# Kernel tuning notes

Hardware: AMD Instinct MI355X
Metric: run time of the kernel (lower is better)

## Reference

```python
import jax, jax.numpy as jnp
import numpy as np

NT, C, B, N, H, E = 32768, 128, 64, 512, 4, 524288  # total nodes, channels, graphs, nodes/graph, heads, edges
DH = C // H
EPS = 1e-5


def batchnorm(x, g, b):
    # BatchNorm1d over the node dimension (training-mode batch statistics)
    m = x.mean(axis=0)
    v = x.var(axis=0)
    return (x - m) * jax.lax.rsqrt(v + EPS) * g + b


def setup_inputs() -> dict:
    key = jax.random.key(0)
    ks = jax.random.split(key, 8)
    s = 1.0 / np.sqrt(C)
    return dict(
        x=jax.random.normal(ks[0], (NT, C), jnp.float32),
        edge_index=jax.random.randint(ks[1], (2, E), 0, NT, dtype=jnp.int32),
        Wc=jax.random.normal(ks[2], (C, C), jnp.float32) * s,
        bc=jnp.zeros((C,), jnp.float32),
        in_proj_w=jax.random.normal(ks[3], (3 * C, C), jnp.float32) * s,
        in_proj_b=jnp.zeros((3 * C,), jnp.float32),
        out_proj_w=jax.random.normal(ks[4], (C, C), jnp.float32) * s,
        out_proj_b=jnp.zeros((C,), jnp.float32),
        gn1=jnp.ones((C,), jnp.float32), bn1=jnp.zeros((C,), jnp.float32),
        gn2=jnp.ones((C,), jnp.float32), bn2=jnp.zeros((C,), jnp.float32),
        gn3=jnp.ones((C,), jnp.float32), bn3=jnp.zeros((C,), jnp.float32),
        Wm1=jax.random.normal(ks[5], (2 * C, C), jnp.float32) * s,
        bm1=jnp.zeros((2 * C,), jnp.float32),
        Wm2=jax.random.normal(ks[6], (C, 2 * C), jnp.float32) / np.sqrt(2 * C),
        bm2=jnp.zeros((C,), jnp.float32),
    )


def reference(x, edge_index, Wc, bc, in_proj_w, in_proj_b, out_proj_w, out_proj_b,
              gn1, bn1, gn2, bn2, gn3, bn3, Wm1, bm1, Wm2, bm2):
    # --- local branch: mean-aggregation message passing + linear + residual + BN ---
    src, dst = edge_index[0], edge_index[1]
    agg = jax.ops.segment_sum(x[src], dst, num_segments=NT)            # [NT, C]
    cnt = jax.ops.segment_sum(jnp.ones((E, 1), x.dtype), dst, num_segments=NT)
    agg = agg / jnp.maximum(cnt, 1.0)
    h_local = agg @ Wc.T + bc + x                                       # dropout p=0 -> no-op
    h_local = batchnorm(h_local, gn1, bn1)

    # --- global branch: to_dense_batch (equal-size graphs -> reshape) + MHA ---
    hd = x.reshape(B, N, C)
    qkv = hd @ in_proj_w.T + in_proj_b                                  # [B, N, 3C]
    q, k, v = jnp.split(qkv, 3, axis=-1)
    q = q.reshape(B, N, H, DH).transpose(0, 2, 1, 3)                    # [B, H, N, DH]
    k = k.reshape(B, N, H, DH).transpose(0, 2, 1, 3)
    v = v.reshape(B, N, H, DH).transpose(0, 2, 1, 3)
    scores = jnp.einsum('bhqd,bhkd->bhqk', q, k) / np.sqrt(DH)          # [B, H, N, N]
    attn = jax.nn.softmax(scores, axis=-1)
    o = jnp.einsum('bhqk,bhkd->bhqd', attn, v)                          # [B, H, N, DH]
    o = o.transpose(0, 2, 1, 3).reshape(B, N, C)
    h_attn = (o @ out_proj_w.T + out_proj_b).reshape(NT, C) + x
    h_attn = batchnorm(h_attn, gn2, bn2)

    # --- combine + MLP + final norm ---
    out = h_local + h_attn
    out = out + (jax.nn.relu(out @ Wm1.T + bm1) @ Wm2.T + bm2)
    return batchnorm(out, gn3, bn3)
```

## Files before the change

kernel.cpp:

```cpp
#include <hip/hip_runtime.h>
#include <cstddef>

#define NT    32768
#define CCH   128
#define BB    64
#define NNODE 512
#define NHEAD 4
#define DHEAD 32
#define EE    524288
#define EPS   1e-5f
#define MAXDEG 96

typedef unsigned short u16;
typedef unsigned int   u32;
typedef __attribute__((ext_vector_type(8))) short short8;
typedef __attribute__((ext_vector_type(4))) short short4v;
typedef __attribute__((ext_vector_type(4))) float f32x4;

__device__ __forceinline__ float b2f(u32 w) { return __uint_as_float(w << 16); }
__device__ __forceinline__ u16 f2b(float f) {
    u32 u = __float_as_uint(f);
    u += 0x7FFF + ((u >> 16) & 1);
    return (u16)(u >> 16);
}

__global__ __launch_bounds__(256) void prep_kernel(const float* __restrict__ x,
                                                   const float* __restrict__ Wc,
                                                   const float* __restrict__ Wqkv,
                                                   const float* __restrict__ Wo,
                                                   const float* __restrict__ Wm1,
                                                   const float* __restrict__ Wm2,
                                                   u16* __restrict__ xb,
                                                   u16* __restrict__ Wcb,
                                                   u16* __restrict__ Wqkvb,
                                                   u16* __restrict__ Wob,
                                                   u16* __restrict__ Wm1b,
                                                   u16* __restrict__ Wm2b,
                                                   const int* __restrict__ ei,
                                                   int* __restrict__ cursor,
                                                   int* __restrict__ bucket) {
    if (blockIdx.x >= 2120) {
        int e = (blockIdx.x - 2120) * 256 + threadIdx.x;
        int src = ei[e];
        int dst = ei[EE + e];
        int pos = atomicAdd(cursor + dst, 1);
        if (pos < MAXDEG) bucket[dst * MAXDEG + pos] = src;
        return;
    }
    int r = blockIdx.x * 256 + threadIdx.x;
    const float* src; u16* dst;
    if (r < 524288) { src = x; dst = xb; }
    else if ((r -= 524288) < 2048) { src = Wc; dst = Wcb; }
    else if ((r -= 2048) < 6144) { src = Wqkv; dst = Wqkvb; }
    else if ((r -= 6144) < 2048) { src = Wo; dst = Wob; }
    else if ((r -= 2048) < 4096) { src = Wm1; dst = Wm1b; }
    else { r -= 4096; src = Wm2; dst = Wm2b; }
    size_t base = (size_t)r * 8;
    float4 a = *(const float4*)(src + base);
    float4 b = *(const float4*)(src + base + 4);
    uint4 u;
    u.x = (u32)f2b(a.x) | ((u32)f2b(a.y) << 16);
    u.y = (u32)f2b(a.z) | ((u32)f2b(a.w) << 16);
    u.z = (u32)f2b(b.x) | ((u32)f2b(b.y) << 16);
    u.w = (u32)f2b(b.z) | ((u32)f2b(b.w) << 16);
    *(uint4*)(dst + base) = u;
}

__global__ __launch_bounds__(256) void stage2_kernel(const int* __restrict__ bucket,
                                                     const int* __restrict__ cursor,
                                                     const u16* __restrict__ xb,
                                                     u16* __restrict__ aggb,
                                                     const u16* __restrict__ Wqkvb,
                                                     const float* __restrict__ bqkv,
                                                     u16* __restrict__ qkvb) {
    __shared__ __align__(16) char smem[26624];
    int tid = threadIdx.x;
    if (blockIdx.x < 4096) {
        int* srcs = (int*)smem;
        int ln = tid >> 5;
        int c4 = tid & 31;
        int n = blockIdx.x * 8 + ln;
        int d = min(cursor[n], MAXDEG);
        for (int j = c4; j < d; j += 32) srcs[ln * MAXDEG + j] = bucket[n * MAXDEG + j];
        __syncthreads();
        float s0 = 0.f, s1 = 0.f, s2 = 0.f, s3 = 0.f;
        for (int j = 0; j < d; ++j) {
            uint2 w = *(const uint2*)(xb + (size_t)srcs[ln * MAXDEG + j] * CCH + c4 * 4);
            s0 += b2f(w.x & 0xffffu);
            s1 += b2f(w.x >> 16);
            s2 += b2f(w.y & 0xffffu);
            s3 += b2f(w.y >> 16);
        }
        float inv = 1.0f / fmaxf((float)d, 1.0f);
        uint2 out;
        out.x = (u32)f2b(s0 * inv) | ((u32)f2b(s1 * inv) << 16);
        out.y = (u32)f2b(s2 * inv) | ((u32)f2b(s3 * inv) << 16);
        *(uint2*)(aggb + (size_t)n * CCH + c4 * 4) = out;
        return;
    }
    int bx = blockIdx.x - 4096;
    int y = bx >> 8;
    int m0 = (bx & 255) * 128;
    const u16* W = Wqkvb + (size_t)y * 128 * 128;
    const float* bias = bqkv + y * 128;
    u16* As = (u16*)smem;
    u16* Bs = (u16*)(smem + 8192);
    u16* Cs = (u16*)(smem + 16384);

    int lane = tid & 63, wave = tid >> 6;
    int wm = (wave & 1) * 64, wn = (wave >> 1) * 64;
    int l15 = lane & 15, l4 = lane >> 4;

    f32x4 zero = {0.f, 0.f, 0.f, 0.f};
    f32x4 acc[4][4];
#pragma unroll
    for (int i = 0; i < 4; ++i)
#pragma unroll
        for (int j = 0; j < 4; ++j) acc[i][j] = zero;

    int srow = tid >> 2;
    int scol = (tid & 3) * 8;

    uint4 a0 = *(const uint4*)(xb + (size_t)(m0 + srow) * 128 + scol);
    uint4 a1 = *(const uint4*)(xb + (size_t)(m0 + srow + 64) * 128 + scol);
    uint4 b0 = *(const uint4*)(W + (size_t)srow * 128 + scol);
    uint4 b1 = *(const uint4*)(W + (size_t)(srow + 64) * 128 + scol);
    for (int ki = 0; ki < 4; ++ki) {
        if (ki) __syncthreads();
        *(uint4*)&As[srow * 32 + scol] = a0;
        *(uint4*)&As[(srow + 64) * 32 + scol] = a1;
        *(uint4*)&Bs[srow * 32 + scol] = b0;
        *(uint4*)&Bs[(srow + 64) * 32 + scol] = b1;
        if (ki < 3) {
            int k0 = (ki + 1) * 32;
            a0 = *(const uint4*)(xb + (size_t)(m0 + srow) * 128 + k0 + scol);
            a1 = *(const uint4*)(xb + (size_t)(m0 + srow + 64) * 128 + k0 + scol);
            b0 = *(const uint4*)(W + (size_t)srow * 128 + k0 + scol);
            b1 = *(const uint4*)(W + (size_t)(srow + 64) * 128 + k0 + scol);
        }
        __syncthreads();
        short8 af[4], bf[4];
#pragma unroll
        for (int t = 0; t < 4; ++t) {
            af[t] = *(const short8*)&As[(wm + t * 16 + l15) * 32 + l4 * 8];
            bf[t] = *(const short8*)&Bs[(wn + t * 16 + l15) * 32 + l4 * 8];
        }
#pragma unroll
        for (int mt = 0; mt < 4; ++mt)
#pragma unroll
            for (int nt = 0; nt < 4; ++nt)
                acc[mt][nt] = __builtin_amdgcn_mfma_f32_16x16x32_bf16(af[mt], bf[nt], acc[mt][nt], 0, 0, 0);
    }

    int rl = lane >> 3;
    int cg = lane & 7;
    u16* Cw = Cs + wave * 16 * 72;
#pragma unroll
    for (int mt = 0; mt < 4; ++mt) {
#pragma unroll
        for (int nt = 0; nt < 4; ++nt) {
            float bs = bias[wn + nt * 16 + l15];
#pragma unroll
            for (int r = 0; r < 4; ++r)
                Cw[(l4 * 4 + r) * 72 + nt * 16 + l15] = f2b(acc[mt][nt][r] + bs);
        }
#pragma unroll
        for (int p = 0; p < 2; ++p) {
            int lrow = p * 8 + rl;
            uint4 wv = *(const uint4*)&Cw[lrow * 72 + cg * 8];
            int grow = m0 + wm + mt * 16 + lrow;
            *(uint4*)(qkvb + (size_t)grow * 384 + y * 128 + wn + cg * 8) = wv;
        }
    }
}

__global__ __launch_bounds__(256) void stage3_kernel(const u16* __restrict__ qkvb,
                                                     u16* __restrict__ ob,
                                                     const u16* __restrict__ aggb,
                                                     const u16* __restrict__ Wcb,
                                                     const float* __restrict__ bc,
                                                     const u16* __restrict__ xb,
                                                     u16* __restrict__ hlocb,
                                                     float* __restrict__ sum1,
                                                     float* __restrict__ sq1) {
    __shared__ __align__(16) char smem[74240];
    int tid = threadIdx.x;
    int lane = tid & 63, wave = tid >> 6;
    int quad = lane >> 4, l15 = lane & 15, l4 = lane >> 4;

    if (blockIdx.x < 256) {
        u16* Ks = (u16*)smem;
        u16* Vt = (u16*)(smem + 40960);
        int bh = blockIdx.x;
        int b = bh >> 2, h = bh & 3;
        const float scale = 0.1767766952966369f;

        const u16* kvbase = qkvb + (size_t)b * 512 * 384 + 128 + h * 32;
        for (int idx = tid; idx < 2048; idx += 256) {
            int row = idx >> 2, c = idx & 3;
            *(uint4*)&Ks[row * 40 + c * 8] = *(const uint4*)(kvbase + (size_t)row * 384 + c * 8);
        }
        for (int idx = tid; idx < 2048; idx += 256) {
            int row = idx >> 2, c = idx & 3;
            uint4 u = *(const uint4*)(kvbase + 128 + (size_t)row * 384 + c * 8);
            u16 e[8];
            *(uint4*)e = u;
#pragma unroll
            for (int i = 0; i < 8; ++i) Vt[(c * 8 + i) * 520 + row] = e[i];
        }
        __syncthreads();

        f32x4 zero = {0.f, 0.f, 0.f, 0.f};
        for (int qt = 0; qt < 8; ++qt) {
            int qbase = wave * 128 + qt * 16;
            short8 qf = *(const short8*)(qkvb + (size_t)(b * 512 + qbase + l15) * 384 + h * 32 + quad * 8);
            float lq = 0.f;
            f32x4 oa[2] = {zero, zero};

            for (int kv0 = 0; kv0 < 512; kv0 += 64) {
                f32x4 s[4];
#pragma unroll
                for (int t = 0; t < 4; ++t) {
                    short8 kb = *(const short8*)&Ks[(kv0 + t * 16 + l15) * 40 + quad * 8];
                    s[t] = __builtin_amdgcn_mfma_f32_16x16x32_bf16(kb, qf, zero, 0, 0, 0);
                }
                short8 pa[4];
#pragma unroll
                for (int t = 0; t < 4; ++t) {
                    float p0 = __expf(s[t][0] * scale);
                    float p1 = __expf(s[t][1] * scale);
                    float p2 = __expf(s[t][2] * scale);
                    float p3 = __expf(s[t][3] * scale);
                    lq += (p0 + p1) + (p2 + p3);
                    short8 a8 = {(short)f2b(p0), (short)f2b(p1), (short)f2b(p2), (short)f2b(p3), 0, 0, 0, 0};
                    pa[t] = a8;
                }
#pragma unroll
                for (int t = 0; t < 4; ++t) {
                    int tbase = kv0 + t * 16;
#pragma unroll
                    for (int n = 0; n < 2; ++n) {
                        short4v v4 = *(const short4v*)&Vt[(n * 16 + l15) * 520 + tbase + quad * 4];
                        short8 vb = {v4.x, v4.y, v4.z, v4.w, 0, 0, 0, 0};
                        oa[n] = __builtin_amdgcn_mfma_f32_16x16x32_bf16(pa[t], vb, oa[n], 0, 0, 0);
                    }
                }
            }
            lq += __shfl_xor(lq, 16);
            lq += __shfl_xor(lq, 32);
            u16* op = ob + (size_t)(b * 512 + qbase) * 128 + h * 32;
#pragma unroll
            for (int r = 0; r < 4; ++r) {
                float Lr = __shfl(lq, quad * 4 + r);
                float inv = 1.0f / Lr;
#pragma unroll
                for (int n = 0; n < 2; ++n)
                    op[(quad * 4 + r) * 128 + n * 16 + l15] = f2b(oa[n][r] * inv);
            }
        }
        return;
    }

    int m0 = (blockIdx.x - 256) * 128;
    u16* As = (u16*)smem;
    u16* Bs = (u16*)(smem + 8192);
    u16* Cs = (u16*)(smem + 16384);
    float* csum = (float*)(smem + 25600);
    float* csq  = (float*)(smem + 26112);
    int wm = (wave & 1) * 64, wn = (wave >> 1) * 64;

    if (tid < 128) { csum[tid] = 0.f; csq[tid] = 0.f; }

    f32x4 zero = {0.f, 0.f, 0.f, 0.f};
    f32x4 acc[4][4];
#pragma unroll
    for (int i = 0; i < 4; ++i)
#pragma unroll
        for (int j = 0; j < 4; ++j) acc[i][j] = zero;

    int srow = tid >> 2;
    int scol = (tid & 3) * 8;

    uint4 a0 = *(const uint4*)(aggb + (size_t)(m0 + srow) * 128 + scol);
    uint4 a1 = *(const uint4*)(aggb + (size_t)(m0 + srow + 64) * 128 + scol);
    uint4 b0 = *(const uint4*)(Wcb + (size_t)srow * 128 + scol);
    uint4 b1 = *(const uint4*)(Wcb + (size_t)(srow + 64) * 128 + scol);
    for (int ki = 0; ki < 4; ++ki) {
        if (ki) __syncthreads();
        *(uint4*)&As[srow * 32 + scol] = a0;
        *(uint4*)&As[(srow + 64) * 32 + scol] = a1;
        *(uint4*)&Bs[srow * 32 + scol] = b0;
        *(uint4*)&Bs[(srow + 64) * 32 + scol] = b1;
        if (ki < 3) {
            int k0 = (ki + 1) * 32;
            a0 = *(const uint4*)(aggb + (size_t)(m0 + srow) * 128 + k0 + scol);
            a1 = *(const uint4*)(aggb + (size_t)(m0 + srow + 64) * 128 + k0 + scol);
            b0 = *(const uint4*)(Wcb + (size_t)srow * 128 + k0 + scol);
            b1 = *(const uint4*)(Wcb + (size_t)(srow + 64) * 128 + k0 + scol);
        }
        __syncthreads();
        short8 af[4], bf[4];
#pragma unroll
        for (int t = 0; t < 4; ++t) {
            af[t] = *(const short8*)&As[(wm + t * 16 + l15) * 32 + l4 * 8];
            bf[t] = *(const short8*)&Bs[(wn + t * 16 + l15) * 32 + l4 * 8];
        }
#pragma unroll
        for (int mt = 0; mt < 4; ++mt)
#pragma unroll
            for (int nt = 0; nt < 4; ++nt)
                acc[mt][nt] = __builtin_amdgcn_mfma_f32_16x16x32_bf16(af[mt], bf[nt], acc[mt][nt], 0, 0, 0);
    }

    float ps[4] = {0.f, 0.f, 0.f, 0.f};
    float pq[4] = {0.f, 0.f, 0.f, 0.f};
    int rl = lane >> 3;
    int cg = lane & 7;
    u16* Cw = Cs + wave * 16 * 72;
#pragma unroll
    for (int mt = 0; mt < 4; ++mt) {
#pragma unroll
        for (int nt = 0; nt < 4; ++nt) {
            int lcol = wn + nt * 16 + l15;
            float bs = bc[lcol];
#pragma unroll
            for (int r = 0; r < 4; ++r) {
                int row = m0 + wm + mt * 16 + l4 * 4 + r;
                float v = acc[mt][nt][r] + bs + b2f(xb[(size_t)row * 128 + lcol]);
                Cw[(l4 * 4 + r) * 72 + nt * 16 + l15] = f2b(v);
                ps[nt] += v; pq[nt] += v * v;
            }
        }
#pragma unroll
        for (int p = 0; p < 2; ++p) {
            int lrow = p * 8 + rl;
            uint4 wv = *(const uint4*)&Cw[lrow * 72 + cg * 8];
            int grow = m0 + wm + mt * 16 + lrow;
            *(uint4*)(hlocb + (size_t)grow * 128 + wn + cg * 8) = wv;
        }
    }
#pragma unroll
    for (int nt = 0; nt < 4; ++nt) {
        atomicAdd(&csum[wn + nt * 16 + l15], ps[nt]);
        atomicAdd(&csq[wn + nt * 16 + l15], pq[nt]);
    }
    __syncthreads();
    if (tid < 128) {
        atomicAdd(sum1 + tid, csum[tid]);
        atomicAdd(sq1 + tid, csq[tid]);
    }
}

template <bool RELU, int RESID, bool STATS>
__global__ __launch_bounds__(256) void gemm_mfma(const u16* __restrict__ A,
                                                 const u16* __restrict__ W,
                                                 const float* __restrict__ bias,
                                                 const u16* __restrict__ residb,
                                                 u16* __restrict__ outb,
                                                 float* __restrict__ sum,
                                                 float* __restrict__ sumsq,
                                                 int M, int N, int K) {
    __shared__ u16 As[128 * 32];
    __shared__ u16 Bs[128 * 32];
    __shared__ u16 Cs[4][16 * 72];
    __shared__ float csum[128];
    __shared__ float csq[128];
    int m0 = blockIdx.x * 128, n0 = blockIdx.y * 128;
    int tid = threadIdx.x;
    int lane = tid & 63, wave = tid >> 6;
    int wm = (wave & 1) * 64, wn = (wave >> 1) * 64;
    int l15 = lane & 15, l4 = lane >> 4;

    if (STATS) {
        if (tid < 128) { csum[tid] = 0.f; csq[tid] = 0.f; }
    }

    f32x4 zero = {0.f, 0.f, 0.f, 0.f};
    f32x4 acc[4][4];
#pragma unroll
    for (int i = 0; i < 4; ++i)
#pragma unroll
        for (int j = 0; j < 4; ++j) acc[i][j] = zero;

    int srow = tid >> 2;
    int scol = (tid & 3) * 8;

    int kIter = K >> 5;
    uint4 a0 = *(const uint4*)(A + (size_t)(m0 + srow) * K + scol);
    uint4 a1 = *(const uint4*)(A + (size_t)(m0 + srow + 64) * K + scol);
    uint4 b0 = *(const uint4*)(W + (size_t)(n0 + srow) * K + scol);
    uint4 b1 = *(const uint4*)(W + (size_t)(n0 + srow + 64) * K + scol);
    for (int ki = 0; ki < kIter; ++ki) {
        if (ki) __syncthreads();
        *(uint4*)&As[srow * 32 + scol] = a0;
        *(uint4*)&As[(srow + 64) * 32 + scol] = a1;
        *(uint4*)&Bs[srow * 32 + scol] = b0;
        *(uint4*)&Bs[(srow + 64) * 32 + scol] = b1;
        if (ki + 1 < kIter) {
            int k0 = (ki + 1) * 32;
            a0 = *(const uint4*)(A + (size_t)(m0 + srow) * K + k0 + scol);
            a1 = *(const uint4*)(A + (size_t)(m0 + srow + 64) * K + k0 + scol);
            b0 = *(const uint4*)(W + (size_t)(n0 + srow) * K + k0 + scol);
            b1 = *(const uint4*)(W + (size_t)(n0 + srow + 64) * K + k0 + scol);
        }
        __syncthreads();
        short8 af[4], bf[4];
#pragma unroll
        for (int t = 0; t < 4; ++t) {
            af[t] = *(const short8*)&As[(wm + t * 16 + l15) * 32 + l4 * 8];
            bf[t] = *(const short8*)&Bs[(wn + t * 16 + l15) * 32 + l4 * 8];
        }
#pragma unroll
        for (int mt = 0; mt < 4; ++mt)
#pragma unroll
            for (int nt = 0; nt < 4; ++nt)
                acc[mt][nt] = __builtin_amdgcn_mfma_f32_16x16x32_bf16(af[mt], bf[nt], acc[mt][nt], 0, 0, 0);
    }

    float ps[4] = {0.f, 0.f, 0.f, 0.f};
    float pq[4] = {0.f, 0.f, 0.f, 0.f};
    int rl = lane >> 3;
    int cg = lane & 7;
#pragma unroll
    for (int mt = 0; mt < 4; ++mt) {
#pragma unroll
        for (int nt = 0; nt < 4; ++nt) {
            int col = n0 + wn + nt * 16 + l15;
            float bs = bias[col];
#pragma unroll
            for (int r = 0; r < 4; ++r) {
                int row = m0 + wm + mt * 16 + l4 * 4 + r;
                float v = acc[mt][nt][r] + bs;
                if (RESID == 2) v += b2f(residb[(size_t)row * N + col]);
                if (RELU) v = fmaxf(v, 0.0f);
                Cs[wave][(l4 * 4 + r) * 72 + nt * 16 + l15] = f2b(v);
                if (STATS) { ps[nt] += v; pq[nt] += v * v; }
            }
        }
#pragma unroll
        for (int p = 0; p < 2; ++p) {
            int lrow = p * 8 + rl;
            uint4 wv = *(const uint4*)&Cs[wave][lrow * 72 + cg * 8];
            int grow = m0 + wm + mt * 16 + lrow;
            *(uint4*)(outb + (size_t)grow * N + n0 + wn + cg * 8) = wv;
        }
    }
    if (STATS) {
#pragma unroll
        for (int nt = 0; nt < 4; ++nt) {
            atomicAdd(&csum[wn + nt * 16 + l15], ps[nt]);
            atomicAdd(&csq[wn + nt * 16 + l15], pq[nt]);
        }
        __syncthreads();
        if (tid < 128) {
            atomicAdd(sum + n0 + tid, csum[tid]);
            atomicAdd(sumsq + n0 + tid, csq[tid]);
        }
    }
}

__global__ __launch_bounds__(256) void gemm_m1c(const u16* __restrict__ hlocb,
                                                const u16* __restrict__ t2b,
                                                const float* __restrict__ sum1,
                                                const float* __restrict__ sq1,
                                                const float* __restrict__ g1,
                                                const float* __restrict__ bt1,
                                                const float* __restrict__ sum2,
                                                const float* __restrict__ sq2,
                                                const float* __restrict__ g2,
                                                const float* __restrict__ bt2,
                                                u16* __restrict__ shb,
                                                const u16* __restrict__ Wm1b,
                                                const float* __restrict__ bm1,
                                                u16* __restrict__ hidb) {
    __shared__ u16 As[128 * 32];
    __shared__ u16 Bs[128 * 32];
    __shared__ u16 Cs[4][16 * 72];
    __shared__ float AF1[128], BF1[128], AF2[128], BF2[128];
    int tid = threadIdx.x;
    {
        int c = tid & 127;
        const float* sm = (tid < 128) ? sum1 : sum2;
        const float* sq = (tid < 128) ? sq1 : sq2;
        const float* g  = (tid < 128) ? g1 : g2;
        const float* bt = (tid < 128) ? bt1 : bt2;
        float m = sm[c] * (1.0f / NT);
        float v = sq[c] * (1.0f / NT) - m * m;
        float a = g[c] * rsqrtf(v + EPS);
        if (tid < 128) { AF1[c] = a; BF1[c] = bt[c] - m * a; }
        else           { AF2[c] = a; BF2[c] = bt[c] - m * a; }
    }
    int m0 = blockIdx.x * 128, n0 = blockIdx.y * 128;
    int lane = tid & 63, wave = tid >> 6;
    int wm = (wave & 1) * 64, wn = (wave >> 1) * 64;
    int l15 = lane & 15, l4 = lane >> 4;

    f32x4 zero = {0.f, 0.f, 0.f, 0.f};
    f32x4 acc[4][4];
#pragma unroll
    for (int i = 0; i < 4; ++i)
#pragma unroll
        for (int j = 0; j < 4; ++j) acc[i][j] = zero;

    int srow = tid >> 2;
    int scol = (tid & 3) * 8;
    bool wr = (blockIdx.y == 0);

    uint4 h0 = *(const uint4*)(hlocb + (size_t)(m0 + srow) * 128 + scol);
    uint4 h1 = *(const uint4*)(hlocb + (size_t)(m0 + srow + 64) * 128 + scol);
    uint4 t0 = *(const uint4*)(t2b + (size_t)(m0 + srow) * 128 + scol);
    uint4 t1 = *(const uint4*)(t2b + (size_t)(m0 + srow + 64) * 128 + scol);
    uint4 b0 = *(const uint4*)(Wm1b + (size_t)(n0 + srow) * 128 + scol);
    uint4 b1 = *(const uint4*)(Wm1b + (size_t)(n0 + srow + 64) * 128 + scol);
    __syncthreads();
    for (int ki = 0; ki < 4; ++ki) {
        int k0 = ki * 32;
        if (ki) __syncthreads();
        uint4 c0, c1;
        {
            const u32 hw[4] = {h0.x, h0.y, h0.z, h0.w};
            const u32 tw[4] = {t0.x, t0.y, t0.z, t0.w};
            u32 ow[4];
#pragma unroll
            for (int p = 0; p < 4; ++p) {
                int cc = k0 + scol + p * 2;
                float v0 = AF1[cc] * b2f(hw[p] & 0xffffu) + BF1[cc] + AF2[cc] * b2f(tw[p] & 0xffffu) + BF2[cc];
                float v1 = AF1[cc + 1] * b2f(hw[p] >> 16) + BF1[cc + 1] + AF2[cc + 1] * b2f(tw[p] >> 16) + BF2[cc + 1];
                ow[p] = (u32)f2b(v0) | ((u32)f2b(v1) << 16);
            }
            c0.x = ow[0]; c0.y = ow[1]; c0.z = ow[2]; c0.w = ow[3];
        }
        {
            const u32 hw[4] = {h1.x, h1.y, h1.z, h1.w};
            const u32 tw[4] = {t1.x, t1.y, t1.z, t1.w};
            u32 ow[4];
#pragma unroll
            for (int p = 0; p < 4; ++p) {
                int cc = k0 + scol + p * 2;
                float v0 = AF1[cc] * b2f(hw[p] & 0xffffu) + BF1[cc] + AF2[cc] * b2f(tw[p] & 0xffffu) + BF2[cc];
                float v1 = AF1[cc + 1] * b2f(hw[p] >> 16) + BF1[cc + 1] + AF2[cc + 1] * b2f(tw[p] >> 16) + BF2[cc + 1];
                ow[p] = (u32)f2b(v0) | ((u32)f2b(v1) << 16);
            }
            c1.x = ow[0]; c1.y = ow[1]; c1.z = ow[2]; c1.w = ow[3];
        }
        *(uint4*)&As[srow * 32 + scol] = c0;
        *(uint4*)&As[(srow + 64) * 32 + scol] = c1;
        *(uint4*)&Bs[srow * 32 + scol] = b0;
        *(uint4*)&Bs[(srow + 64) * 32 + scol] = b1;
        if (wr) {
            *(uint4*)(shb + (size_t)(m0 + srow) * 128 + k0 + scol) = c0;
            *(uint4*)(shb + (size_t)(m0 + srow + 64) * 128 + k0 + scol) = c1;
        }
        if (ki < 3) {
            int kn = k0 + 32;
            h0 = *(const uint4*)(hlocb + (size_t)(m0 + srow) * 128 + kn + scol);
            h1 = *(const uint4*)(hlocb + (size_t)(m0 + srow + 64) * 128 + kn + scol);
            t0 = *(const uint4*)(t2b + (size_t)(m0 + srow) * 128 + kn + scol);
            t1 = *(const uint4*)(t2b + (size_t)(m0 + srow + 64) * 128 + kn + scol);
            b0 = *(const uint4*)(Wm1b + (size_t)(n0 + srow) * 128 + kn + scol);
            b1 = *(const uint4*)(Wm1b + (size_t)(n0 + srow + 64) * 128 + kn + scol);
        }
        __syncthreads();
        short8 af[4], bf[4];
#pragma unroll
        for (int t = 0; t < 4; ++t) {
            af[t] = *(const short8*)&As[(wm + t * 16 + l15) * 32 + l4 * 8];
            bf[t] = *(const short8*)&Bs[(wn + t * 16 + l15) * 32 + l4 * 8];
        }
#pragma unroll
        for (int mt = 0; mt < 4; ++mt)
#pragma unroll
            for (int nt = 0; nt < 4; ++nt)
                acc[mt][nt] = __builtin_amdgcn_mfma_f32_16x16x32_bf16(af[mt], bf[nt], acc[mt][nt], 0, 0, 0);
    }

    int rl = lane >> 3;
    int cg = lane & 7;
#pragma unroll
    for (int mt = 0; mt < 4; ++mt) {
#pragma unroll
        for (int nt = 0; nt < 4; ++nt) {
            int col = n0 + wn + nt * 16 + l15;
            float bs = bm1[col];
#pragma unroll
            for (int r = 0; r < 4; ++r) {
                float v = fmaxf(acc[mt][nt][r] + bs, 0.0f);
                Cs[wave][(l4 * 4 + r) * 72 + nt * 16 + l15] = f2b(v);
            }
        }
#pragma unroll
        for (int p = 0; p < 2; ++p) {
            int lrow = p * 8 + rl;
            uint4 wv = *(const uint4*)&Cs[wave][lrow * 72 + cg * 8];
            int grow = m0 + wm + mt * 16 + lrow;
            *(uint4*)(hidb + (size_t)grow * 256 + n0 + wn + cg * 8) = wv;
        }
    }
}

__global__ __launch_bounds__(256) void final_bn(const u16* __restrict__ X,
                                                const float* __restrict__ sum3,
                                                const float* __restrict__ sq3,
                                                const float* __restrict__ g3,
                                                const float* __restrict__ bt3,
                                                float* __restrict__ outp) {
    __shared__ float A3[128], B3[128];
    int t = threadIdx.x;
    if (t < 128) {
        float m = sum3[t] * (1.0f / NT);
        float v = sq3[t] * (1.0f / NT) - m * m;
        float a = g3[t] * rsqrtf(v + EPS);
        A3[t] = a;
        B3[t] = bt3[t] - m * a;
    }
    __syncthreads();
    int i8 = blockIdx.x * 256 + t;
    size_t i = (size_t)i8 * 8;
    int c = (int)(i & (CCH - 1));
    uint4 u = *(const uint4*)(X + i);
    float x[8];
    x[0] = b2f(u.x & 0xffffu); x[1] = b2f(u.x >> 16);
    x[2] = b2f(u.y & 0xffffu); x[3] = b2f(u.y >> 16);
    x[4] = b2f(u.z & 0xffffu); x[5] = b2f(u.z >> 16);
    x[6] = b2f(u.w & 0xffffu); x[7] = b2f(u.w >> 16);
    float4 o0, o1;
    o0.x = A3[c + 0] * x[0] + B3[c + 0];
    o0.y = A3[c + 1] * x[1] + B3[c + 1];
    o0.z = A3[c + 2] * x[2] + B3[c + 2];
    o0.w = A3[c + 3] * x[3] + B3[c + 3];
    o1.x = A3[c + 4] * x[4] + B3[c + 4];
    o1.y = A3[c + 5] * x[5] + B3[c + 5];
    o1.z = A3[c + 6] * x[6] + B3[c + 6];
    o1.w = A3[c + 7] * x[7] + B3[c + 7];
    *(float4*)(outp + i) = o0;
    *(float4*)(outp + i + 4) = o1;
}

extern "C" void kernel_launch(void* const* d_in, const int* in_sizes, int n_in,
                              void* d_out, int out_size, void* d_ws, size_t ws_size,
                              hipStream_t stream) {
    const float* x    = (const float*)d_in[0];
    const int*   ei   = (const int*)d_in[1];
    const float* Wc   = (const float*)d_in[2];
    const float* bc   = (const float*)d_in[3];
    const float* Wqkv = (const float*)d_in[4];
    const float* bqkv = (const float*)d_in[5];
    const float* Wo   = (const float*)d_in[6];
    const float* bo   = (const float*)d_in[7];
    const float* gn1  = (const float*)d_in[8];
    const float* bn1b = (const float*)d_in[9];
    const float* gn2  = (const float*)d_in[10];
    const float* bn2b = (const float*)d_in[11];
    const float* gn3  = (const float*)d_in[12];
    const float* bn3b = (const float*)d_in[13];
    const float* Wm1  = (const float*)d_in[14];
    const float* bm1  = (const float*)d_in[15];
    const float* Wm2  = (const float*)d_in[16];
    const float* bm2  = (const float*)d_in[17];
    float* outp = (float*)d_out;

    char* w = (char*)d_ws;
    const size_t MB = 1024 * 1024;
    u16* xb    = (u16*)(w);
    u16* hlocb = (u16*)(w + 8 * MB);
    u16* t2b   = (u16*)(w + 16 * MB);
    u16* out2b = (u16*)(w + 24 * MB);
    u16* qkvb  = (u16*)(w + 32 * MB);
    u16* hidb  = (u16*)(w + 56 * MB);
    u16* shb   = (u16*)(w + 72 * MB);
    int* bucket = (int*)(w + 80 * MB);
    int* cursor = (int*)(w + 92 * MB);
    float* stats = (float*)(w + 92 * MB + 128 * 1024);
    u16* Wcb   = (u16*)(w + 93 * MB);
    u16* Wqkvb = Wcb + 16384;
    u16* Wob   = Wqkvb + 49152;
    u16* Wm1b  = Wob + 16384;
    u16* Wm2b  = Wm1b + 32768;
    u16* ob    = (u16*)(w + 94 * MB);
    float* sum1 = stats;        float* sq1 = stats + 128;
    float* sum2 = stats + 256;  float* sq2 = stats + 384;
    float* sum3 = stats + 512;  float* sq3 = stats + 640;

    hipMemsetAsync(cursor, 0, 128 * 1024 + 6 * 128 * 4, stream);

    prep_kernel<<<2120 + 2048, 256, 0, stream>>>(x, Wc, Wqkv, Wo, Wm1, Wm2,
                                                 xb, Wcb, Wqkvb, Wob, Wm1b, Wm2b,
                                                 ei, cursor, bucket);

    stage2_kernel<<<4096 + 768, 256, 0, stream>>>(bucket, cursor, xb, shb,
                                                  Wqkvb, bqkv, qkvb);

    stage3_kernel<<<512, 256, 0, stream>>>(qkvb, ob, shb, Wcb, bc, xb,
                                           hlocb, sum1, sq1);

    {
        dim3 g(NT / 128, 1);
        gemm_mfma<false, 2, true><<<g, 256, 0, stream>>>(
            ob, Wob, bo, xb, t2b, sum2, sq2, NT, 128, 128);
    }

    {
        dim3 g(NT / 128, 2);
        gemm_m1c<<<g, 256, 0, stream>>>(hlocb, t2b, sum1, sq1, gn1, bn1b,
                                        sum2, sq2, gn2, bn2b, shb, Wm1b, bm1, hidb);
    }

    {
        dim3 g(NT / 128, 1);
        gemm_mfma<false, 2, true><<<g, 256, 0, stream>>>(
            hidb, Wm2b, bm2, shb, out2b, sum3, sq3, NT, 128, 256);
    }

    final_bn<<<NT * CCH / 8 / 256, 256, 0, stream>>>(out2b, sum3, sq3, gn3, bn3b, outp);
}
```

Baseline: 257.5 us.

## Regroup kernel stages: overlap bucket fill with QKV, aggregation with attention

Restructures the cross-kernel schedule. Edge bucketing now runs in the same launch as the QKV projection (4 edges per thread, u16 source indices). Neighbor aggregation is co-scheduled with attention in a 512-thread kernel, and the Wc and Wo projections are merged into one two-column GEMM launch. The aim is better overlap of latency-bound gather and atomic work with MFMA work, plus lower bucket memory traffic. Storing indices as u16 truncates node ids above 65535, but NT is 32768 so they fit. The larger block size and changed Vt padding may alter occupancy and bank conflicts in attention.

After: 252.7 us. About the same (-1.9%).

```diff
diff --git a/kernel.cpp b/kernel.cpp
--- a/kernel.cpp
+++ b/kernel.cpp
@@ -10,6 +10,7 @@
 #define EE    524288
 #define EPS   1e-5f
 #define MAXDEG 96
+#define VTS   524
 
 typedef unsigned short u16;
 typedef unsigned int   u32;
@@ -24,29 +25,18 @@
     return (u16)(u >> 16);
 }
 
-__global__ __launch_bounds__(256) void prep_kernel(const float* __restrict__ x,
-                                                   const float* __restrict__ Wc,
-                                                   const float* __restrict__ Wqkv,
-                                                   const float* __restrict__ Wo,
-                                                   const float* __restrict__ Wm1,
-                                                   const float* __restrict__ Wm2,
-                                                   u16* __restrict__ xb,
-                                                   u16* __restrict__ Wcb,
-                                                   u16* __restrict__ Wqkvb,
-                                                   u16* __restrict__ Wob,
-                                                   u16* __restrict__ Wm1b,
-                                                   u16* __restrict__ Wm2b,
-                                                   const int* __restrict__ ei,
-                                                   int* __restrict__ cursor,
-                                                   int* __restrict__ bucket) {
-    if (blockIdx.x >= 2120) {
-        int e = (blockIdx.x - 2120) * 256 + threadIdx.x;
-        int src = ei[e];
-        int dst = ei[EE + e];
-        int pos = atomicAdd(cursor + dst, 1);
-        if (pos < MAXDEG) bucket[dst * MAXDEG + pos] = src;
-        return;
-    }
+__global__ __launch_bounds__(256) void convert_kernel(const float* __restrict__ x,
+                                                      const float* __restrict__ Wc,
+                                                      const float* __restrict__ Wqkv,
+                                                      const float* __restrict__ Wo,
+                                                      const float* __restrict__ Wm1,
+                                                      const float* __restrict__ Wm2,
+                                                      u16* __restrict__ xb,
+                                                      u16* __restrict__ Wcb,
+                                                      u16* __restrict__ Wqkvb,
+                                                      u16* __restrict__ Wob,
+                                                      u16* __restrict__ Wm1b,
+                                                      u16* __restrict__ Wm2b) {
     int r = blockIdx.x * 256 + threadIdx.x;
     const float* src; u16* dst;
     if (r < 524288) { src = x; dst = xb; }
@@ -66,39 +56,31 @@
     *(uint4*)(dst + base) = u;
 }
 
-__global__ __launch_bounds__(256) void stage2_kernel(const int* __restrict__ bucket,
-                                                     const int* __restrict__ cursor,
-                                                     const u16* __restrict__ xb,
-                                                     u16* __restrict__ aggb,
-                                                     const u16* __restrict__ Wqkvb,
-                                                     const float* __restrict__ bqkv,
-                                                     u16* __restrict__ qkvb) {
-    __shared__ __align__(16) char smem[26624];
+__global__ __launch_bounds__(256) void fill_qkv_kernel(const int* __restrict__ ei,
+                                                       int* __restrict__ cursor,
+                                                       u16* __restrict__ bucket,
+                                                       const u16* __restrict__ xb,
+                                                       const u16* __restrict__ Wqkvb,
+                                                       const float* __restrict__ bqkv,
+                                                       u16* __restrict__ qkvb) {
+    __shared__ __align__(16) char smem[25600];
     int tid = threadIdx.x;
-    if (blockIdx.x < 4096) {
-        int* srcs = (int*)smem;
-        int ln = tid >> 5;
-        int c4 = tid & 31;
-        int n = blockIdx.x * 8 + ln;
-        int d = min(cursor[n], MAXDEG);
-        for (int j = c4; j < d; j += 32) srcs[ln * MAXDEG + j] = bucket[n * MAXDEG + j];
-        __syncthreads();
-        float s0 = 0.f, s1 = 0.f, s2 = 0.f, s3 = 0.f;
-        for (int j = 0; j < d; ++j) {
-            uint2 w = *(const uint2*)(xb + (size_t)srcs[ln * MAXDEG + j] * CCH + c4 * 4);
-            s0 += b2f(w.x & 0xffffu);
-            s1 += b2f(w.x >> 16);
-            s2 += b2f(w.y & 0xffffu);
-            s3 += b2f(w.y >> 16);
-        }
-        float inv = 1.0f / fmaxf((float)d, 1.0f);
-        uint2 out;
-        out.x = (u32)f2b(s0 * inv) | ((u32)f2b(s1 * inv) << 16);
-        out.y = (u32)f2b(s2 * inv) | ((u32)f2b(s3 * inv) << 16);
-        *(uint2*)(aggb + (size_t)n * CCH + c4 * 4) = out;
+    if (blockIdx.x >= 768) {
+        int t = (blockIdx.x - 768) * 256 + tid;
+        int e = t * 4;
+        int4 sv = *(const int4*)(ei + e);
+        int4 dv = *(const int4*)(ei + EE + e);
+        int p0 = atomicAdd(cursor + dv.x, 1);
+        int p1 = atomicAdd(cursor + dv.y, 1);
+        int p2 = atomicAdd(cursor + dv.z, 1);
+        int p3 = atomicAdd(cursor + dv.w, 1);
+        if (p0 < MAXDEG) bucket[dv.x * MAXDEG + p0] = (u16)sv.x;
+        if (p1 < MAXDEG) bucket[dv.y * MAXDEG + p1] = (u16)sv.y;
+        if (p2 < MAXDEG) bucket[dv.z * MAXDEG + p2] = (u16)sv.z;
+        if (p3 < MAXDEG) bucket[dv.w * MAXDEG + p3] = (u16)sv.w;
         return;
     }
-    int bx = blockIdx.x - 4096;
+    int bx = blockIdx.x;
     int y = bx >> 8;
     int m0 = (bx & 255) * 128;
     const u16* W = Wqkvb + (size_t)y * 128 * 128;
@@ -174,100 +156,141 @@
     }
 }
 
-__global__ __launch_bounds__(256) void stage3_kernel(const u16* __restrict__ qkvb,
-                                                     u16* __restrict__ ob,
-                                                     const u16* __restrict__ aggb,
-                                                     const u16* __restrict__ Wcb,
-                                                     const float* __restrict__ bc,
-                                                     const u16* __restrict__ xb,
-                                                     u16* __restrict__ hlocb,
-                                                     float* __restrict__ sum1,
-                                                     float* __restrict__ sq1) {
-    __shared__ __align__(16) char smem[74240];
+__global__ __launch_bounds__(512) void agg_attn_kernel(const u16* __restrict__ qkvb,
+                                                       u16* __restrict__ ob,
+                                                       const u16* __restrict__ bucket,
+                                                       const int* __restrict__ cursor,
+                                                       const u16* __restrict__ xb,
+                                                       u16* __restrict__ aggb) {
+    __shared__ __align__(16) char smem[74496];
+    int tid = threadIdx.x;
+    if (blockIdx.x >= 256) {
+        int* srcs = (int*)smem;
+        int ln = tid >> 5;
+        int c4 = tid & 31;
+        int n = (blockIdx.x - 256) * 16 + ln;
+        int d = min(cursor[n], MAXDEG);
+        for (int j = c4; j < d; j += 32) srcs[ln * MAXDEG + j] = bucket[n * MAXDEG + j];
+        __syncthreads();
+        float s0 = 0.f, s1 = 0.f, s2 = 0.f, s3 = 0.f;
+        for (int j = 0; j < d; ++j) {
+            uint2 w = *(const uint2*)(xb + (size_t)srcs[ln * MAXDEG + j] * CCH + c4 * 4);
+            s0 += b2f(w.x & 0xffffu);
+            s1 += b2f(w.x >> 16);
+            s2 += b2f(w.y & 0xffffu);
+            s3 += b2f(w.y >> 16);
+        }
+        float inv = 1.0f / fmaxf((float)d, 1.0f);
+        uint2 out;
+        out.x = (u32)f2b(s0 * inv) | ((u32)f2b(s1 * inv) << 16);
+        out.y = (u32)f2b(s2 * inv) | ((u32)f2b(s3 * inv) << 16);
+        *(uint2*)(aggb + (size_t)n * CCH + c4 * 4) = out;
+        return;
+    }
+    u16* Ks = (u16*)smem;
+    u16* Vt = (u16*)(smem + 40960);
+    int bh = blockIdx.x;
+    int b = bh >> 2, h = bh & 3;
+    int lane = tid & 63, wave = tid >> 6;
+    int quad = lane >> 4, l15 = lane & 15;
+    const float scale = 0.1767766952966369f;
+
+    const u16* kvbase = qkvb + (size_t)b * 512 * 384 + 128 + h * 32;
+    for (int idx = tid; idx < 2048; idx += 512) {
+        int row = idx >> 2, c = idx & 3;
+        *(uint4*)&Ks[row * 40 + c * 8] = *(const uint4*)(kvbase + (size_t)row * 384 + c * 8);
+    }
+    for (int idx = tid; idx < 2048; idx += 512) {
+        int row = idx >> 2, c = idx & 3;
+        uint4 u = *(const uint4*)(kvbase + 128 + (size_t)row * 384 + c * 8);
+        u16 e[8];
+        *(uint4*)e = u;
+#pragma unroll
+        for (int i = 0; i < 8; ++i) Vt[(c * 8 + i) * VTS + row] = e[i];
+    }
+    __syncthreads();
+
+    f32x4 zero = {0.f, 0.f, 0.f, 0.f};
+    for (int qt = 0; qt < 4; ++qt) {
+        int qbase = wave * 64 + qt * 16;
+        short8 qf = *(const short8*)(qkvb + (size_t)(b * 512 + qbase + l15) * 384 + h * 32 + quad * 8);
+        float lq = 0.f;
+        f32x4 oa[2] = {zero, zero};
+
+        for (int kv0 = 0; kv0 < 512; kv0 += 64) {
+            f32x4 s[4];
+#pragma unroll
+            for (int t = 0; t < 4; ++t) {
+                short8 kb = *(const short8*)&Ks[(kv0 + t * 16 + l15) * 40 + quad * 8];
+                s[t] = __builtin_amdgcn_mfma_f32_16x16x32_bf16(kb, qf, zero, 0, 0, 0);
+            }
+            short8 pa[4];
+#pragma unroll
+            for (int t = 0; t < 4; ++t) {
+                float p0 = __expf(s[t][0] * scale);
+                float p1 = __expf(s[t][1] * scale);
+                float p2 = __expf(s[t][2] * scale);
+                float p3 = __expf(s[t][3] * scale);
+                lq += (p0 + p1) + (p2 + p3);
+                short8 a8 = {(short)f2b(p0), (short)f2b(p1), (short)f2b(p2), (short)f2b(p3), 0, 0, 0, 0};
+                pa[t] = a8;
+            }
+#pragma unroll
+            for (int t = 0; t < 4; ++t) {
+                int tbase = kv0 + t * 16;
+#pragma unroll
+                for (int n = 0; n < 2; ++n) {
+                    short4v v4 = *(const short4v*)&Vt[(n * 16 + l15) * VTS + tbase + quad * 4];
+                    short8 vb = {v4.x, v4.y, v4.z, v4.w, 0, 0, 0, 0};
+                    oa[n] = __builtin_amdgcn_mfma_f32_16x16x32_bf16(pa[t], vb, oa[n], 0, 0, 0);
+                }
+            }
+        }
+        lq += __shfl_xor(lq, 16);
+        lq += __shfl_xor(lq, 32);
+        u16* op = ob + (size_t)(b * 512 + qbase) * 128 + h * 32;
+#pragma unroll
+        for (int r = 0; r < 4; ++r) {
+            float Lr = __shfl(lq, quad * 4 + r);
+            float inv = 1.0f / Lr;
+#pragma unroll
+            for (int n = 0; n < 2; ++n)
+                op[(quad * 4 + r) * 128 + n * 16 + l15] = f2b(oa[n][r] * inv);
+        }
+    }
+}
+
+__global__ __launch_bounds__(256) void gemm_wcwo(const u16* __restrict__ aggb,
+                                                 const u16* __restrict__ ob,
+                                                 const u16* __restrict__ Wcb,
+                                                 const u16* __restrict__ Wob,
+                                                 const float* __restrict__ bc,
+                                                 const float* __restrict__ bo,
+                                                 const u16* __restrict__ xb,
+                                                 u16* __restrict__ hlocb,
+                                                 u16* __restrict__ t2b,
+                                                 float* __restrict__ sum1,
+                                                 float* __restrict__ sq1,
+                                                 float* __restrict__ sum2,
+                                                 float* __restrict__ sq2) {
+    __shared__ u16 As[128 * 32];
+    __shared__ u16 Bs[128 * 32];
+    __shared__ u16 Cs[4][16 * 72];
+    __shared__ float csum[128];
+    __shared__ float csq[128];
+    int y = blockIdx.y;
+    const u16* A = y ? ob : aggb;
+    const u16* W = y ? Wob : Wcb;
+    const float* bias = y ? bo : bc;
+    u16* outb = y ? t2b : hlocb;
+    float* sum = y ? sum2 : sum1;
+    float* sumsq = y ? sq2 : sq1;
+
+    int m0 = blockIdx.x * 128;
     int tid = threadIdx.x;
     int lane = tid & 63, wave = tid >> 6;
-    int quad = lane >> 4, l15 = lane & 15, l4 = lane >> 4;
-
-    if (blockIdx.x < 256) {
-        u16* Ks = (u16*)smem;
-        u16* Vt = (u16*)(smem + 40960);
-        int bh = blockIdx.x;
-        int b = bh >> 2, h = bh & 3;
-        const float scale = 0.1767766952966369f;
-
-        const u16* kvbase = qkvb + (size_t)b * 512 * 384 + 128 + h * 32;
-        for (int idx = tid; idx < 2048; idx += 256) {
-            int row = idx >> 2, c = idx & 3;
-            *(uint4*)&Ks[row * 40 + c * 8] = *(const uint4*)(kvbase + (size_t)row * 384 + c * 8);
-        }
-        for (int idx = tid; idx < 2048; idx += 256) {
-            int row = idx >> 2, c = idx & 3;
-            uint4 u = *(const uint4*)(kvbase + 128 + (size_t)row * 384 + c * 8);
-            u16 e[8];
-            *(uint4*)e = u;
-#pragma unroll
-            for (int i = 0; i < 8; ++i) Vt[(c * 8 + i) * 520 + row] = e[i];
-        }
-        __syncthreads();
-
-        f32x4 zero = {0.f, 0.f, 0.f, 0.f};
-        for (int qt = 0; qt < 8; ++qt) {
-            int qbase = wave * 128 + qt * 16;
-            short8 qf = *(const short8*)(qkvb + (size_t)(b * 512 + qbase + l15) * 384 + h * 32 + quad * 8);
-            float lq = 0.f;
-            f32x4 oa[2] = {zero, zero};
-
-            for (int kv0 = 0; kv0 < 512; kv0 += 64) {
-                f32x4 s[4];
-#pragma unroll
-                for (int t = 0; t < 4; ++t) {
-                    short8 kb = *(const short8*)&Ks[(kv0 + t * 16 + l15) * 40 + quad * 8];
-                    s[t] = __builtin_amdgcn_mfma_f32_16x16x32_bf16(kb, qf, zero, 0, 0, 0);
-                }
-                short8 pa[4];
-#pragma unroll
-                for (int t = 0; t < 4; ++t) {
-                    float p0 = __expf(s[t][0] * scale);
-                    float p1 = __expf(s[t][1] * scale);
-                    float p2 = __expf(s[t][2] * scale);
-                    float p3 = __expf(s[t][3] * scale);
-                    lq += (p0 + p1) + (p2 + p3);
-                    short8 a8 = {(short)f2b(p0), (short)f2b(p1), (short)f2b(p2), (short)f2b(p3), 0, 0, 0, 0};
-                    pa[t] = a8;
-                }
-#pragma unroll
-                for (int t = 0; t < 4; ++t) {
-                    int tbase = kv0 + t * 16;
-#pragma unroll
-                    for (int n = 0; n < 2; ++n) {
-                        short4v v4 = *(const short4v*)&Vt[(n * 16 + l15) * 520 + tbase + quad * 4];
-                        short8 vb = {v4.x, v4.y, v4.z, v4.w, 0, 0, 0, 0};
-                        oa[n] = __builtin_amdgcn_mfma_f32_16x16x32_bf16(pa[t], vb, oa[n], 0, 0, 0);
-                    }
-                }
-            }
-            lq += __shfl_xor(lq, 16);
-            lq += __shfl_xor(lq, 32);
-            u16* op = ob + (size_t)(b * 512 + qbase) * 128 + h * 32;
-#pragma unroll
-            for (int r = 0; r < 4; ++r) {
-                float Lr = __shfl(lq, quad * 4 + r);
-                float inv = 1.0f / Lr;
-#pragma unroll
-                for (int n = 0; n < 2; ++n)
-                    op[(quad * 4 + r) * 128 + n * 16 + l15] = f2b(oa[n][r] * inv);
-            }
-        }
-        return;
-    }
-
-    int m0 = (blockIdx.x - 256) * 128;
-    u16* As = (u16*)smem;
-    u16* Bs = (u16*)(smem + 8192);
-    u16* Cs = (u16*)(smem + 16384);
-    float* csum = (float*)(smem + 25600);
-    float* csq  = (float*)(smem + 26112);
     int wm = (wave & 1) * 64, wn = (wave >> 1) * 64;
+    int l15 = lane & 15, l4 = lane >> 4;
 
     if (tid < 128) { csum[tid] = 0.f; csq[tid] = 0.f; }
 
@@ -281,10 +304,10 @@
     int srow = tid >> 2;
     int scol = (tid & 3) * 8;
 
-    uint4 a0 = *(const uint4*)(aggb + (size_t)(m0 + srow) * 128 + scol);
-    uint4 a1 = *(const uint4*)(aggb + (size_t)(m0 + srow + 64) * 128 + scol);
-    uint4 b0 = *(const uint4*)(Wcb + (size_t)srow * 128 + scol);
-    uint4 b1 = *(const uint4*)(Wcb + (size_t)(srow + 64) * 128 + scol);
+    uint4 a0 = *(const uint4*)(A + (size_t)(m0 + srow) * 128 + scol);
+    uint4 a1 = *(const uint4*)(A + (size_t)(m0 + srow + 64) * 128 + scol);
+    uint4 b0 = *(const uint4*)(W + (size_t)srow * 128 + scol);
+    uint4 b1 = *(const uint4*)(W + (size_t)(srow + 64) * 128 + scol);
     for (int ki = 0; ki < 4; ++ki) {
         if (ki) __syncthreads();
         *(uint4*)&As[srow * 32 + scol] = a0;
@@ -293,10 +316,10 @@
         *(uint4*)&Bs[(srow + 64) * 32 + scol] = b1;
         if (ki < 3) {
             int k0 = (ki + 1) * 32;
-            a0 = *(const uint4*)(aggb + (size_t)(m0 + srow) * 128 + k0 + scol);
-            a1 = *(const uint4*)(aggb + (size_t)(m0 + srow + 64) * 128 + k0 + scol);
-            b0 = *(const uint4*)(Wcb + (size_t)srow * 128 + k0 + scol);
-            b1 = *(const uint4*)(Wcb + (size_t)(srow + 64) * 128 + k0 + scol);
+            a0 = *(const uint4*)(A + (size_t)(m0 + srow) * 128 + k0 + scol);
+            a1 = *(const uint4*)(A + (size_t)(m0 + srow + 64) * 128 + k0 + scol);
+            b0 = *(const uint4*)(W + (size_t)srow * 128 + k0 + scol);
+            b1 = *(const uint4*)(W + (size_t)(srow + 64) * 128 + k0 + scol);
         }
         __syncthreads();
         short8 af[4], bf[4];
@@ -316,27 +339,26 @@
     float pq[4] = {0.f, 0.f, 0.f, 0.f};
     int rl = lane >> 3;
     int cg = lane & 7;
-    u16* Cw = Cs + wave * 16 * 72;
 #pragma unroll
     for (int mt = 0; mt < 4; ++mt) {
 #pragma unroll
         for (int nt = 0; nt < 4; ++nt) {
             int lcol = wn + nt * 16 + l15;
-            float bs = bc[lcol];
+            float bs = bias[lcol];
 #pragma unroll
             for (int r = 0; r < 4; ++r) {
                 int row = m0 + wm + mt * 16 + l4 * 4 + r;
                 float v = acc[mt][nt][r] + bs + b2f(xb[(size_t)row * 128 + lcol]);
-                Cw[(l4 * 4 + r) * 72 + nt * 16 + l15] = f2b(v);
+                Cs[wave][(l4 * 4 + r) * 72 + nt * 16 + l15] = f2b(v);
                 ps[nt] += v; pq[nt] += v * v;
             }
         }
 #pragma unroll
         for (int p = 0; p < 2; ++p) {
             int lrow = p * 8 + rl;
-            uint4 wv = *(const uint4*)&Cw[lrow * 72 + cg * 8];
+            uint4 wv = *(const uint4*)&Cs[wave][lrow * 72 + cg * 8];
             int grow = m0 + wm + mt * 16 + lrow;
-            *(uint4*)(hlocb + (size_t)grow * 128 + wn + cg * 8) = wv;
+            *(uint4*)(outb + (size_t)grow * 128 + wn + cg * 8) = wv;
         }
     }
 #pragma unroll
@@ -346,8 +368,8 @@
     }
     __syncthreads();
     if (tid < 128) {
-        atomicAdd(sum1 + tid, csum[tid]);
-        atomicAdd(sq1 + tid, csq[tid]);
+        atomicAdd(sum + tid, csum[tid]);
+        atomicAdd(sumsq + tid, csq[tid]);
     }
 }
 
@@ -668,7 +690,7 @@
     u16* qkvb  = (u16*)(w + 32 * MB);
     u16* hidb  = (u16*)(w + 56 * MB);
     u16* shb   = (u16*)(w + 72 * MB);
-    int* bucket = (int*)(w + 80 * MB);
+    u16* bucket = (u16*)(w + 80 * MB);
     int* cursor = (int*)(w + 92 * MB);
     float* stats = (float*)(w + 92 * MB + 128 * 1024);
     u16* Wcb   = (u16*)(w + 93 * MB);
@@ -683,20 +705,18 @@
 
     hipMemsetAsync(cursor, 0, 128 * 1024 + 6 * 128 * 4, stream);
 
-    prep_kernel<<<2120 + 2048, 256, 0, stream>>>(x, Wc, Wqkv, Wo, Wm1, Wm2,
-                                                 xb, Wcb, Wqkvb, Wob, Wm1b, Wm2b,
-                                                 ei, cursor, bucket);
-
-    stage2_kernel<<<4096 + 768, 256, 0, stream>>>(bucket, cursor, xb, shb,
-                                                  Wqkvb, bqkv, qkvb);
-
-    stage3_kernel<<<512, 256, 0, stream>>>(qkvb, ob, shb, Wcb, bc, xb,
-                                           hlocb, sum1, sq1);
+    convert_kernel<<<2120, 256, 0, stream>>>(x, Wc, Wqkv, Wo, Wm1, Wm2,
+                                             xb, Wcb, Wqkvb, Wob, Wm1b, Wm2b);
+
+    fill_qkv_kernel<<<768 + 512, 256, 0, stream>>>(ei, cursor, bucket,
+                                                   xb, Wqkvb, bqkv, qkvb);
+
+    agg_attn_kernel<<<256 + 2048, 512, 0, stream>>>(qkvb, ob, bucket, cursor, xb, shb);
 
     {
-        dim3 g(NT / 128, 1);
-        gemm_mfma<false, 2, true><<<g, 256, 0, stream>>>(
-            ob, Wob, bo, xb, t2b, sum2, sq2, NT, 128, 128);
+        dim3 g(NT / 128, 2);
+        gemm_wcwo<<<g, 256, 0, stream>>>(shb, ob, Wcb, Wob, bc, bo, xb,
+                                         hlocb, t2b, sum1, sq1, sum2, sq2);
     }
 
     {
```
